# Kernel tuning notes

Hardware: AMD Instinct MI355X
Metric: run time of the kernel (lower is better)

## Reference

```python
import jax, jax.numpy as jnp
import numpy as np

C = 128  # n_atom_basis


def setup_inputs() -> dict:
    key = jax.random.key(0)
    k_h, k_A, k_Ww, k_Wb, k_aw, k_ab = jax.random.split(key, 6)
    B, N = 8, 2048
    h = jax.random.normal(k_h, (B, N, C), dtype=jnp.float32)
    A = jax.random.uniform(k_A, (B, N, N), dtype=jnp.float32)
    # nn.Linear(C, C)
    lim_W = 1.0 / np.sqrt(C)
    W_w = jax.random.uniform(k_Ww, (C, C), minval=-lim_W, maxval=lim_W, dtype=jnp.float32)
    W_b = jax.random.uniform(k_Wb, (C,), minval=-lim_W, maxval=lim_W, dtype=jnp.float32)
    # nn.Linear(2C, 1)
    lim_a = 1.0 / np.sqrt(2 * C)
    a_w = jax.random.uniform(k_aw, (2 * C,), minval=-lim_a, maxval=lim_a, dtype=jnp.float32)
    a_b = jax.random.uniform(k_ab, (), minval=-lim_a, maxval=lim_a, dtype=jnp.float32)
    return {"h": h, "A": A, "W_w": W_w, "W_b": W_b, "a_w": a_w, "a_b": a_b}


def reference(h, A, W_w, W_b, a_w, a_b):
    # Wh computed once ([B,N,C]) instead of the original's redundant [B,N,N,C] broadcast.
    Wh = jnp.einsum('bnc,dc->bnd', h, W_w) + W_b
    # a([hi, hj]) = a_w[:C]@Wh_i + a_w[C:]@Wh_j + a_b  -> rank-1 decomposition of the concat-linear
    si = Wh @ a_w[:C]          # [B,N]
    sj = Wh @ a_w[C:]          # [B,N]
    s = si[:, :, None] + sj[:, None, :] + a_b  # [B,N,N] raw scores
    e = jnp.exp(s) * A                          # masked exp (no max-subtraction: matches original math)
    alpha = e / jnp.sum(e, axis=2, keepdims=True)
    # weighted sum over neighbors j of the ORIGINAL h (as in the source, not Wh)
    h_prime = jnp.einsum('bij,bjc->bic', alpha, h)
    return h_prime
```

## Files before the change

### kernel.cpp

```cpp
#include <hip/hip_runtime.h>
#include <math.h>
#include <stdint.h>

#define Bn 8
#define Nn 2048
#define Cn 128
#define CP 144
#define NKB (Nn / 32)

typedef _Float16 f16x8 __attribute__((ext_vector_type(8)));
typedef _Float16 f16x2 __attribute__((ext_vector_type(2)));
typedef __fp16   fp16x2 __attribute__((ext_vector_type(2)));
typedef float    f32x4 __attribute__((ext_vector_type(4)));

__device__ __forceinline__ void dma16(const void* g, void* l) {
    __builtin_amdgcn_global_load_lds((const __attribute__((address_space(1))) uint32_t*)g,
                                     (__attribute__((address_space(3))) uint32_t*)l,
                                     16, 0, 0);
}

__global__ __launch_bounds__(256) void rows_kernel(const float* __restrict__ h,
                                                   const float* __restrict__ Ww,
                                                   const float* __restrict__ Wb,
                                                   const float* __restrict__ aw,
                                                   _Float16* __restrict__ hWt) {
    __shared__ float tile[64][132];
    __shared__ float vsh[128];
    __shared__ float vpart[128];
    __shared__ float wsh[64];
    __shared__ float b2sh;

    int bid = blockIdx.x;
    int b   = bid & 7;
    int n0  = (bid >> 3) << 6;
    int tid = threadIdx.x;

    {
        int c = tid & 127, half = tid >> 7;
        float acc = 0.f;
#pragma unroll
        for (int dd = 0; dd < 64; ++dd) {
            int d = half * 64 + dd;
            acc += Ww[d * Cn + c] * aw[Cn + d];
        }
        if (half) vpart[c] = acc; else vsh[c] = acc;
    }
    if (tid < 64) {
        float b2p = Wb[tid] * aw[Cn + tid] + Wb[tid + 64] * aw[Cn + tid + 64];
        b2p += __shfl_xor(b2p, 32, 64);
        b2p += __shfl_xor(b2p, 16, 64);
        b2p += __shfl_xor(b2p, 8, 64);
        b2p += __shfl_xor(b2p, 4, 64);
        b2p += __shfl_xor(b2p, 2, 64);
        b2p += __shfl_xor(b2p, 1, 64);
        if (tid == 0) b2sh = b2p;
    }
    {
        int r = tid >> 2, qq = tid & 3;
        const float4* rowp = (const float4*)(h + (size_t)(b * Nn + n0 + r) * Cn);
#pragma unroll
        for (int i = 0; i < 8; ++i) {
            int f4 = i * 4 + qq;
            *(float4*)&tile[r][f4 * 4] = rowp[f4];
        }
    }
    __syncthreads();

    {
        int r = tid >> 2, pp = tid & 3;
        float acc = 0.f;
#pragma unroll
        for (int ii = 0; ii < 32; ++ii) {
            int i = pp * 32 + ii;
            acc += tile[r][i] * (vsh[i] + vpart[i]);
        }
        acc += __shfl_xor(acc, 1, 64);
        acc += __shfl_xor(acc, 2, 64);
        if (pp == 0) wsh[r] = expf(acc + b2sh);
    }
    __syncthreads();

    _Float16* hWb = hWt + ((size_t)(b * NKB + (n0 >> 5)) * CP) * 32;
#pragma unroll
    for (int i = 0; i < 18; ++i) {
        int idx = tid + 256 * i;
        int cp  = idx >> 5;
        int rem = idx & 31;
        int kbl = rem >> 4, p = rem & 15;
        int ks0 = p * 2;
        int r0  = kbl * 32 + ks0;
        f16x2 v2;
        if (cp < 128) {
            v2[0] = (_Float16)(wsh[r0] * tile[r0][cp]);
            v2[1] = (_Float16)(wsh[r0 + 1] * tile[r0 + 1][cp]);
        } else if (cp == 128) {
            v2[0] = (_Float16)wsh[r0];
            v2[1] = (_Float16)wsh[r0 + 1];
        } else {
            v2[0] = (_Float16)0.f;
            v2[1] = (_Float16)0.f;
        }
        *(f16x2*)(hWb + ((size_t)kbl * CP + cp) * 32 + ks0) = v2;
    }
}

__global__ __launch_bounds__(256, 4) void attn_kernel(const float* __restrict__ A,
                                                      const _Float16* __restrict__ hWt,
                                                      float* __restrict__ out) {
    __shared__ float Alds[2][16 * 64];
    __shared__ float den[16];

    int bid = blockIdx.x;
    int b   = bid & 7;
    int i0  = (bid >> 3) << 4;
    int tid = threadIdx.x;
    int wv  = tid >> 6, l = tid & 63;
    int m   = l & 15, q = l >> 4;

    const float*    Ab  = A   + (size_t)(b * Nn + i0) * Nn;
    const _Float16* hWb = hWt + (size_t)b * NKB * CP * 32;

    int sr = wv * 4 + q;
    int skq = (m - sr) & 15;
    const float* sg = Ab + (size_t)sr * Nn + skq * 4;
    float* sl = &Alds[0][0] + wv * 256;

    f32x4 acc[3];
#pragma unroll
    for (int s = 0; s < 3; ++s) acc[s] = (f32x4){0.f, 0.f, 0.f, 0.f};

    dma16(sg, sl);

    for (int t = 0; t < 32; ++t) {
        int buf = t & 1;
        if (t < 31) dma16(sg + (t + 1) * 64, sl + (buf ^ 1) * (16 * 64));
        __syncthreads();

        f16x8 bf[6];
#pragma unroll
        for (int ksub = 0; ksub < 2; ++ksub)
#pragma unroll
            for (int s = 0; s < 3; ++s) {
                int ct = (s == 2) ? 8 : wv * 2 + s;
                bf[ksub * 3 + s] = *(const f16x8*)(
                    hWb + ((size_t)(t * 2 + ksub) * CP + ct * 16 + m) * 32 + q * 8);
            }
#pragma unroll
        for (int ksub = 0; ksub < 2; ++ksub) {
            int kq0 = ksub * 8 + 2 * q;
            float4 x = *(const float4*)&Alds[buf][m * 64 + ((kq0 + m) & 15) * 4];
            float4 y = *(const float4*)&Alds[buf][m * 64 + ((kq0 + 1 + m) & 15) * 4];
            union { fp16x2 h2[4]; f16x8 v; } u;
            u.h2[0] = __builtin_amdgcn_cvt_pkrtz(x.x, x.y);
            u.h2[1] = __builtin_amdgcn_cvt_pkrtz(x.z, x.w);
            u.h2[2] = __builtin_amdgcn_cvt_pkrtz(y.x, y.y);
            u.h2[3] = __builtin_amdgcn_cvt_pkrtz(y.z, y.w);
#pragma unroll
            for (int s = 0; s < 3; ++s)
                acc[s] = __builtin_amdgcn_mfma_f32_16x16x32_f16(u.v, bf[ksub * 3 + s],
                                                                acc[s], 0, 0, 0);
        }
        __syncthreads();
    }

    if (wv == 0 && m == 0) {
#pragma unroll
        for (int r = 0; r < 4; ++r) den[q * 4 + r] = acc[2][r];
    }
    __syncthreads();

#pragma unroll
    for (int r = 0; r < 4; ++r) {
        float invd = 1.f / den[q * 4 + r];
        float* ob = out + (size_t)(b * Nn + i0 + q * 4 + r) * Cn;
#pragma unroll
        for (int s = 0; s < 2; ++s)
            ob[(wv * 2 + s) * 16 + m] = acc[s][r] * invd;
    }
}

extern "C" void kernel_launch(void* const* d_in, const int* in_sizes, int n_in,
                              void* d_out, int out_size, void* d_ws, size_t ws_size,
                              hipStream_t stream) {
    const float* h  = (const float*)d_in[0];
    const float* A  = (const float*)d_in[1];
    const float* Ww = (const float*)d_in[2];
    const float* Wb = (const float*)d_in[3];
    const float* aw = (const float*)d_in[4];
    float* out = (float*)d_out;

    _Float16* hWt = (_Float16*)d_ws;

    rows_kernel<<<Bn * (Nn / 64), 256, 0, stream>>>(h, Ww, Wb, aw, hWt);
    attn_kernel<<<Bn * (Nn / 16), 256, 0, stream>>>(A, hWt, out);
}
```

Measured before the change: 252.2 us.

## Shrink rows-kernel tiles, stagger K start per block, use one barrier per iteration

The rows kernel now handles 16 rows per block instead of 64, giving four times as many blocks. The attention kernel starts each block's K loop at a staggered offset so that concurrent blocks read different hWt slices, spreading cache and channel traffic. The K loop also drops its trailing barrier by issuing the next DMA after the leading barrier, which leaves one sync per iteration. The trade-off is that each rows block recomputes the Ww·aw vector, so that redundant work is now done four times as often.

After: 242.9 us. 1.04x faster.

```diff
diff --git a/kernel.cpp b/kernel.cpp
--- a/kernel.cpp
+++ b/kernel.cpp
@@ -24,15 +24,15 @@
                                                    const float* __restrict__ Wb,
                                                    const float* __restrict__ aw,
                                                    _Float16* __restrict__ hWt) {
-    __shared__ float tile[64][132];
-    __shared__ float vsh[128];
-    __shared__ float vpart[128];
-    __shared__ float wsh[64];
+    __shared__ float tile[16][132];
+    __shared__ float vlo[128];
+    __shared__ float vhi[128];
+    __shared__ float wsh[16];
     __shared__ float b2sh;
 
     int bid = blockIdx.x;
     int b   = bid & 7;
-    int n0  = (bid >> 3) << 6;
+    int n0  = (bid >> 3) << 4;
     int tid = threadIdx.x;
 
     {
@@ -43,7 +43,7 @@
             int d = half * 64 + dd;
             acc += Ww[d * Cn + c] * aw[Cn + d];
         }
-        if (half) vpart[c] = acc; else vsh[c] = acc;
+        if (half) vhi[c] = acc; else vlo[c] = acc;
     }
     if (tid < 64) {
         float b2p = Wb[tid] * aw[Cn + tid] + Wb[tid + 64] * aw[Cn + tid + 64];
@@ -56,51 +56,55 @@
         if (tid == 0) b2sh = b2p;
     }
     {
-        int r = tid >> 2, qq = tid & 3;
-        const float4* rowp = (const float4*)(h + (size_t)(b * Nn + n0 + r) * Cn);
-#pragma unroll
-        for (int i = 0; i < 8; ++i) {
-            int f4 = i * 4 + qq;
-            *(float4*)&tile[r][f4 * 4] = rowp[f4];
+#pragma unroll
+        for (int i = 0; i < 2; ++i) {
+            int idx = tid + 256 * i;
+            int r = idx >> 5, f4 = idx & 31;
+            *(float4*)&tile[r][f4 * 4] =
+                ((const float4*)(h + (size_t)(b * Nn + n0 + r) * Cn))[f4];
         }
     }
     __syncthreads();
 
     {
-        int r = tid >> 2, pp = tid & 3;
+        int r = tid >> 4, g = tid & 15;
         float acc = 0.f;
 #pragma unroll
-        for (int ii = 0; ii < 32; ++ii) {
-            int i = pp * 32 + ii;
-            acc += tile[r][i] * (vsh[i] + vpart[i]);
+        for (int ii = 0; ii < 8; ++ii) {
+            int i = g * 8 + ii;
+            acc += tile[r][i] * (vlo[i] + vhi[i]);
         }
         acc += __shfl_xor(acc, 1, 64);
         acc += __shfl_xor(acc, 2, 64);
-        if (pp == 0) wsh[r] = expf(acc + b2sh);
+        acc += __shfl_xor(acc, 4, 64);
+        acc += __shfl_xor(acc, 8, 64);
+        if (g == 0) wsh[r] = expf(acc + b2sh);
     }
     __syncthreads();
 
-    _Float16* hWb = hWt + ((size_t)(b * NKB + (n0 >> 5)) * CP) * 32;
-#pragma unroll
-    for (int i = 0; i < 18; ++i) {
-        int idx = tid + 256 * i;
-        int cp  = idx >> 5;
-        int rem = idx & 31;
-        int kbl = rem >> 4, p = rem & 15;
-        int ks0 = p * 2;
-        int r0  = kbl * 32 + ks0;
-        f16x2 v2;
-        if (cp < 128) {
-            v2[0] = (_Float16)(wsh[r0] * tile[r0][cp]);
-            v2[1] = (_Float16)(wsh[r0 + 1] * tile[r0 + 1][cp]);
-        } else if (cp == 128) {
-            v2[0] = (_Float16)wsh[r0];
-            v2[1] = (_Float16)wsh[r0 + 1];
-        } else {
-            v2[0] = (_Float16)0.f;
-            v2[1] = (_Float16)0.f;
-        }
-        *(f16x2*)(hWb + ((size_t)kbl * CP + cp) * 32 + ks0) = v2;
+    {
+        int kb = n0 >> 5, khalf = (n0 >> 4) & 1;
+        _Float16* hWb = hWt + ((size_t)(b * NKB + kb) * CP) * 32 + khalf * 16;
+#pragma unroll
+        for (int i = 0; i < 5; ++i) {
+            int idx = tid + 256 * i;
+            if (idx < 1152) {
+                int cp = idx >> 3, p = idx & 7;
+                int r0 = p * 2;
+                f16x2 v2;
+                if (cp < 128) {
+                    v2[0] = (_Float16)(wsh[r0] * tile[r0][cp]);
+                    v2[1] = (_Float16)(wsh[r0 + 1] * tile[r0 + 1][cp]);
+                } else if (cp == 128) {
+                    v2[0] = (_Float16)wsh[r0];
+                    v2[1] = (_Float16)wsh[r0 + 1];
+                } else {
+                    v2[0] = (_Float16)0.f;
+                    v2[1] = (_Float16)0.f;
+                }
+                *(f16x2*)(hWb + (size_t)cp * 32 + p * 2) = v2;
+            }
+        }
     }
 }
 
@@ -113,6 +117,7 @@
     int bid = blockIdx.x;
     int b   = bid & 7;
     int i0  = (bid >> 3) << 4;
+    int koff = ((bid >> 3) * 5 + (bid & 7)) & 31;
     int tid = threadIdx.x;
     int wv  = tid >> 6, l = tid & 63;
     int m   = l & 15, q = l >> 4;
@@ -120,7 +125,7 @@
     const float*    Ab  = A   + (size_t)(b * Nn + i0) * Nn;
     const _Float16* hWb = hWt + (size_t)b * NKB * CP * 32;
 
-    int sr = wv * 4 + q;
+    int sr  = wv * 4 + q;
     int skq = (m - sr) & 15;
     const float* sg = Ab + (size_t)sr * Nn + skq * 4;
     float* sl = &Alds[0][0] + wv * 256;
@@ -129,13 +134,16 @@
 #pragma unroll
     for (int s = 0; s < 3; ++s) acc[s] = (f32x4){0.f, 0.f, 0.f, 0.f};
 
-    dma16(sg, sl);
+    dma16(sg + (size_t)koff * 64, sl);
 
     for (int t = 0; t < 32; ++t) {
         int buf = t & 1;
-        if (t < 31) dma16(sg + (t + 1) * 64, sl + (buf ^ 1) * (16 * 64));
         __syncthreads();
-
+        if (t < 31)
+            dma16(sg + (size_t)((t + 1 + koff) & 31) * 64,
+                  sl + (buf ^ 1) * (16 * 64));
+
+        int kb = (t + koff) & 31;
         f16x8 bf[6];
 #pragma unroll
         for (int ksub = 0; ksub < 2; ++ksub)
@@ -143,7 +151,7 @@
             for (int s = 0; s < 3; ++s) {
                 int ct = (s == 2) ? 8 : wv * 2 + s;
                 bf[ksub * 3 + s] = *(const f16x8*)(
-                    hWb + ((size_t)(t * 2 + ksub) * CP + ct * 16 + m) * 32 + q * 8);
+                    hWb + ((size_t)(kb * 2 + ksub) * CP + ct * 16 + m) * 32 + q * 8);
             }
 #pragma unroll
         for (int ksub = 0; ksub < 2; ++ksub) {
@@ -160,7 +168,6 @@
                 acc[s] = __builtin_amdgcn_mfma_f32_16x16x32_f16(u.v, bf[ksub * 3 + s],
                                                                 acc[s], 0, 0, 0);
         }
-        __syncthreads();
     }
 
     if (wv == 0 && m == 0) {
@@ -191,6 +198,6 @@
 
     _Float16* hWt = (_Float16*)d_ws;
 
-    rows_kernel<<<Bn * (Nn / 64), 256, 0, stream>>>(h, Ww, Wb, aw, hWt);
+    rows_kernel<<<Bn * (Nn / 16), 256, 0, stream>>>(h, Ww, Wb, aw, hWt);
     attn_kernel<<<Bn * (Nn / 16), 256, 0, stream>>>(A, hWt, out);
 }
```
